# Kernel optimization log

Measured on AMD Instinct MI355X. Metric: run time of the kernel, lower is better.

Reference implementation:

```python
import jax, jax.numpy as jnp
import numpy as np
from functools import partial

V, E, H, F = 32000, 256, 512, 256  # vocab, embed_dim, hidden_dim, num_filters
FS = (3, 4, 5)

def setup_inputs() -> dict:
    key = jax.random.key(0)
    ks = jax.random.split(key, 24)
    s = 0.02
    d = {}
    d["src"] = jax.random.randint(ks[0], (32, 512), 0, V)
    d["trg"] = jax.random.randint(ks[1], (32, 64), 0, V)
    # embeddings with padding_idx=0 zeroed
    d["enc_emb"] = (jax.random.normal(ks[2], (V, E)) * s).at[0].set(0.0)
    d["dec_emb"] = (jax.random.normal(ks[3], (V, E)) * s).at[0].set(0.0)
    # conv1d weights (out_channels=F, in_channels=E, kernel)
    d["conv_w3"] = jax.random.normal(ks[4], (F, E, 3)) * s
    d["conv_b3"] = jnp.zeros((F,))
    d["conv_w4"] = jax.random.normal(ks[5], (F, E, 4)) * s
    d["conv_b4"] = jnp.zeros((F,))
    d["conv_w5"] = jax.random.normal(ks[6], (F, E, 5)) * s
    d["conv_b5"] = jnp.zeros((F,))
    d["fc1_w"] = jax.random.normal(ks[7], (H, 3 * F)) * s
    d["fc1_b"] = jnp.zeros((H,))
    d["fc2_w"] = jax.random.normal(ks[8], (H, H)) * s
    d["fc2_b"] = jnp.zeros((H,))
    # 2-layer LSTM: layer1 input E+H, layer2 input H; gates order i,f,g,o
    d["w_ih1"] = jax.random.normal(ks[9], (4 * H, E + H)) * s
    d["w_hh1"] = jax.random.normal(ks[10], (4 * H, H)) * s
    d["b_ih1"] = jnp.zeros((4 * H,))
    d["b_hh1"] = jnp.zeros((4 * H,))
    d["w_ih2"] = jax.random.normal(ks[11], (4 * H, H)) * s
    d["w_hh2"] = jax.random.normal(ks[12], (4 * H, H)) * s
    d["b_ih2"] = jnp.zeros((4 * H,))
    d["b_hh2"] = jnp.zeros((4 * H,))
    d["out_w"] = jax.random.normal(ks[13], (V, H)) * s
    d["out_b"] = jnp.zeros((V,))
    return d

def _lstm_cell(x, h, c, w_ih, w_hh, b_ih, b_hh):
    gates = x @ w_ih.T + b_ih + h @ w_hh.T + b_hh  # (B, 4H)
    i, f, g, o = jnp.split(gates, 4, axis=-1)
    c_new = jax.nn.sigmoid(f) * c + jax.nn.sigmoid(i) * jnp.tanh(g)
    h_new = jax.nn.sigmoid(o) * jnp.tanh(c_new)
    return h_new, c_new

def _encoder(src, enc_emb, convs, fc1_w, fc1_b, fc2_w, fc2_b):
    x = enc_emb[src]                    # (B, S, E)
    x = jnp.transpose(x, (0, 2, 1))     # (B, E, S)
    pooled = []
    for w, b in convs:
        y = jax.lax.conv_general_dilated(
            x, w, window_strides=(1,), padding='VALID',
            dimension_numbers=('NCH', 'OIH', 'NCH'))  # (B, F, S-k+1)
        pooled.append(jnp.max(jax.nn.relu(y + b[None, :, None]), axis=2))
    cat = jnp.concatenate(pooled, axis=1)              # (B, 3F)
    h = jax.nn.relu(cat @ fc1_w.T + fc1_b)             # (B, H)
    return h @ fc2_w.T + fc2_b                         # (B, H)

def reference(src, trg, enc_emb, conv_w3, conv_b3, conv_w4, conv_b4,
              conv_w5, conv_b5, fc1_w, fc1_b, fc2_w, fc2_b, dec_emb,
              w_ih1, w_hh1, b_ih1, b_hh1, w_ih2, w_hh2, b_ih2, b_hh2,
              out_w, out_b):
    B, T = trg.shape
    enc_out = _encoder(src, enc_emb,
                       [(conv_w3, conv_b3), (conv_w4, conv_b4), (conv_w5, conv_b5)],
                       fc1_w, fc1_b, fc2_w, fc2_b)  # (B, H)

    def step(carry, tok):
        h1, c1, h2, c2 = carry
        x = jnp.concatenate([dec_emb[tok], enc_out], axis=1)  # (B, E+H)
        h1, c1 = _lstm_cell(x, h1, c1, w_ih1, w_hh1, b_ih1, b_hh1)
        h2, c2 = _lstm_cell(h1, h2, c2, w_ih2, w_hh2, b_ih2, b_hh2)
        logits = h2 @ out_w.T + out_b                          # (B, V)
        return (h1, c1, h2, c2), logits

    z = jnp.zeros((B, H), dtype=enc_out.dtype)
    tokens = trg[:, :-1].T  # teacher forcing (ratio=1.0): (T-1, B)
    _, logits = jax.lax.scan(step, (z, z, z, z), tokens)       # (T-1, B, V)
    logits = jnp.transpose(logits, (1, 0, 2))                  # (B, T-1, V)
    # outputs[:, 0] is left as zeros, matching the torch loop starting at t=1
    return jnp.concatenate([jnp.zeros((B, 1, logits.shape[-1]), logits.dtype), logits], axis=1)
```

## Files before the change

kernel.cpp:

```cpp
#include <hip/hip_runtime.h>
#include <math.h>
#include <stdint.h>

#define B_    32
#define E_    256
#define F_    256
#define H_    512
#define V_    32000
#define G4    2048

typedef unsigned short u16;
typedef unsigned long long u64;
typedef __attribute__((ext_vector_type(8))) short bf16x8;
typedef __attribute__((ext_vector_type(4))) float f32x4;

__device__ __forceinline__ float fsig(float x) {
  return __builtin_amdgcn_rcpf(1.f + __expf(-x));
}
__device__ __forceinline__ float ftanh(float x) {
  return 1.f - 2.f * __builtin_amdgcn_rcpf(1.f + __expf(2.f * x));
}

__device__ __forceinline__ u16 f2bf(float f) {
  uint32_t u = __float_as_uint(f);
  uint32_t r = (u + 0x7FFFu + ((u >> 16) & 1u)) >> 16;
  return (u16)r;
}
__device__ __forceinline__ uint32_t pack2(float a, float b) {
  return (uint32_t)f2bf(a) | ((uint32_t)f2bf(b) << 16);
}

#define GLOAD16(gp, lp) __builtin_amdgcn_global_load_lds( \
    (const __attribute__((address_space(1))) uint32_t*)(const void*)(gp), \
    (__attribute__((address_space(3))) uint32_t*)(void*)(lp), 16, 0, 0)

#define ALOAD(P) __hip_atomic_load((P), __ATOMIC_RELAXED, __HIP_MEMORY_SCOPE_AGENT)
#define ASTORE(P, V) __hip_atomic_store((P), (V), __ATOMIC_RELAXED, __HIP_MEMORY_SCOPE_AGENT)

__global__ void prep_all(float* pooled, uint32_t* sent1, uint32_t* sent2,
                         uint32_t* cnt1, u16* h1d, u16* h2a,
                         const float* bi1, const float* bh1,
                         const float* bi2, const float* bh2,
                         float* bs1, float* bs2, float* out,
                         const float* s0, u16* d0, const float* s1, u16* d1,
                         const float* s2, u16* d2, const float* s3, u16* d3,
                         const float* s4, u16* d4,
                         const float* w3, u16* t3, const float* w4, u16* t4,
                         const float* w5, u16* t5) {
  int i = blockIdx.x * blockDim.x + threadIdx.x, st = gridDim.x * blockDim.x;
  for (int k = i; k < 2637824; k += st) {
    int j = k; const float* s; u16* d;
    if (j < 2048000) { s = s0; d = d0; }
    else if ((j -= 2048000) < 196608) { s = s1; d = d1; }
    else if ((j -= 196608) < 131072) { s = s2; d = d2; }
    else if ((j -= 131072) < 131072) { s = s3; d = d3; }
    else { j -= 131072; s = s4; d = d4; }
    const float4* sp = (const float4*)s + 2 * (size_t)j;
    float4 a = sp[0], b = sp[1];
    uint4 u;
    u.x = pack2(a.x, a.y); u.y = pack2(a.z, a.w);
    u.z = pack2(b.x, b.y); u.w = pack2(b.z, b.w);
    *((uint4*)d + j) = u;
  }
  for (int k = i; k < 786432; k += st) {
    int j = k; const float* w; u16* wt; int kw;
    if (j < 196608) { w = w3; wt = t3; kw = 3; }
    else if ((j -= 196608) < 262144) { w = w4; wt = t4; kw = 4; }
    else { j -= 262144; w = w5; wt = t5; kw = 5; }
    int f = j / (kw * 256);
    int r = j - f * (kw * 256);
    int jj = r >> 8, e = r & 255;
    wt[j] = f2bf(w[(f * 256 + e) * kw + jj]);
  }
  for (int k = i; k < 24576; k += st) pooled[k] = 0.f;
  for (int k = i; k < 131072; k += st) {
    uint32_t v = (k < 2048 && (k & 15) == 0) ? 1u : 0u;
    sent1[k] = v; sent2[k] = v;
  }
  for (int k = i; k < 256; k += st) cnt1[k] = 0u;
  uint4 z = {0u, 0u, 0u, 0u};
  for (int k = i; k < 2048; k += st) { ((uint4*)h1d)[k] = z; ((uint4*)h2a)[k] = z; }
  for (int k = i; k < G4; k += st) { bs1[k] = bi1[k] + bh1[k]; bs2[k] = bi2[k] + bh2[k]; }
  for (int k = i; k < B_ * V_; k += st) {
    int b = k / V_, v = k - b * V_;
    __builtin_nontemporal_store(0.f, &out[(size_t)b * 64 * V_ + v]);
  }
}

__global__ void gemm_small(const float* __restrict__ A, const float* __restrict__ W,
                           const float* __restrict__ bias, float* __restrict__ C,
                           int K, int N, int relu) {
  int nl = threadIdx.x & 7, b = threadIdx.x >> 3;
  int n = blockIdx.x * 8 + nl;
  const float* a = A + b * K;
  const float* w = W + (size_t)n * K;
  float acc = 0.f;
  for (int k = 0; k < K; k += 4) {
    float4 av = *reinterpret_cast<const float4*>(&a[k]);
    float4 wv = *reinterpret_cast<const float4*>(&w[k]);
    acc = fmaf(av.x, wv.x, acc); acc = fmaf(av.y, wv.y, acc);
    acc = fmaf(av.z, wv.z, acc); acc = fmaf(av.w, wv.w, acc);
  }
  acc += bias[n];
  if (relu) acc = fmaxf(acc, 0.f);
  C[b * N + n] = acc;
}

__global__ __launch_bounds__(256)
void conv_mfma(const u16* __restrict__ wt3, const u16* __restrict__ wt4,
               const u16* __restrict__ wt5,
               const float* __restrict__ cb3, const float* __restrict__ cb4,
               const float* __restrict__ cb5,
               float* __restrict__ pooled,
               const int* __restrict__ srcTok, const float* __restrict__ emb) {
  const int z = blockIdx.z;
  const u16* Bw = (z == 0) ? wt3 : (z == 1) ? wt4 : wt5;
  const float* bias = (z == 0) ? cb3 : (z == 1) ? cb4 : cb5;
  const int K = 768 + 256 * z, kw = 3 + z, poolOff = 256 * z;

  __shared__ char smem[32768];
  const int tid = threadIdx.x;
  const int wid = tid >> 6, lane = tid & 63;
  const int hi = lane >> 4, lo = lane & 15;
  const int wr = wid >> 1, wc = wid & 1;
  const int m0 = blockIdx.x * 128, n0 = blockIdx.y * 128;
  const int NT = K >> 5;
  const int srow = lane >> 2, sc = lane & 3;

  f32x4 acc[4][4];
#pragma unroll
  for (int i = 0; i < 4; ++i)
#pragma unroll
    for (int j = 0; j < 4; ++j) acc[i][j] = (f32x4){0.f, 0.f, 0.f, 0.f};

  for (int t = -1; t < NT; ++t) {
    int ts = t + 1;
    if (ts < NT) {
      char* base = smem + (ts & 1) * 16384;
      int k0 = ts << 5;
      {
        int j = k0 >> 8, e0 = k0 & 255;
        int row = tid >> 1;
        int m = m0 + row;
        int s = m & 511, b = m >> 9;
        int sj = s + j;
        int tok = (sj < 512) ? srcTok[b * 512 + sj] : -1;
#pragma unroll
        for (int q = 0; q < 2; ++q) {
          int cg = (tid & 1) * 2 + q;
          uint4 u;
          if (tok >= 0) {
            const float* ep = emb + (size_t)tok * 256 + e0 + cg * 8;
            float4 f0 = *(const float4*)(ep);
            float4 f1 = *(const float4*)(ep + 4);
            u.x = pack2(f0.x, f0.y); u.y = pack2(f0.z, f0.w);
            u.z = pack2(f1.x, f1.y); u.w = pack2(f1.z, f1.w);
          } else u = (uint4){0, 0, 0, 0};
          int c = cg ^ (row & 3);
          *(uint4*)(base + row * 64 + c * 16) = u;
        }
      }
#pragma unroll
      for (int q = 0; q < 2; ++q) {
        int row = (wid + q * 4) * 16 + srow;
        int gc = sc ^ (row & 3);
        const char* gp = (const char*)Bw + (((size_t)(n0 + row) * K + k0) << 1) + gc * 16;
        GLOAD16(gp, base + 8192 + (wid + q * 4) * 1024);
      }
    }
    if (t >= 0) {
      char* base = smem + (t & 1) * 16384;
      bf16x8 af[4], bfr[4];
#pragma unroll
      for (int mi = 0; mi < 4; ++mi) {
        int row = wr * 64 + mi * 16 + lo;
        af[mi] = *(const bf16x8*)(base + row * 64 + ((hi ^ (row & 3)) << 4));
      }
#pragma unroll
      for (int ni = 0; ni < 4; ++ni) {
        int row = wc * 64 + ni * 16 + lo;
        bfr[ni] = *(const bf16x8*)(base + 8192 + row * 64 + ((hi ^ (row & 3)) << 4));
      }
#pragma unroll
      for (int mi = 0; mi < 4; ++mi)
#pragma unroll
        for (int ni = 0; ni < 4; ++ni)
          acc[mi][ni] = __builtin_amdgcn_mfma_f32_16x16x32_bf16(af[mi], bfr[ni], acc[mi][ni], 0, 0, 0);
    }
    __syncthreads();
  }

  int b = m0 >> 9;
  int slim = 512 - kw;
#pragma unroll
  for (int ni = 0; ni < 4; ++ni) {
    int col = n0 + wc * 64 + ni * 16 + lo;
    float bv = bias[col];
    float mx = 0.f;
#pragma unroll
    for (int mi = 0; mi < 4; ++mi)
#pragma unroll
      for (int r = 0; r < 4; ++r) {
        int m = m0 + wr * 64 + mi * 16 + hi * 4 + r;
        int s = m & 511;
        float v = acc[mi][ni][r] + bv;
        if (s <= slim && v > mx) mx = v;
      }
    atomicMax((int*)&pooled[b * 768 + poolOff + col], __float_as_int(mx));
  }
}

__global__ __launch_bounds__(256, 1)
void lstm_fused(float* __restrict__ pre,
                const u16* __restrict__ whh1,
                const u16* __restrict__ wih2, const u16* __restrict__ whh2,
                const float* __restrict__ bs2,
                uint32_t* __restrict__ sent1, uint32_t* __restrict__ sent2,
                uint32_t* __restrict__ cnt1,
                u16* __restrict__ h1d, u16* __restrict__ h2a,
                const u16* __restrict__ outw_bf, const float* __restrict__ outb,
                float* __restrict__ out,
                const int* __restrict__ trg, const float* __restrict__ demb,
                const float* __restrict__ enco,
                const u16* __restrict__ wih1_bf, const float* __restrict__ bs1) {
  __shared__ char smem[74752];
  const int tid = threadIdx.x;
  const int wid = tid >> 6, lane = tid & 63, hi = lane >> 4, lo = lane & 15;
  const int hrow = tid >> 3, k8 = tid & 7;
  const int pb = hrow, pj0 = k8 * 2;

#define WAVE_DRAIN() asm volatile("s_waitcnt vmcnt(0)" ::: "memory")
#define POLL1(P) while (ALOAD(P) == 0u) __builtin_amdgcn_s_sleep(1);
#define POLL2(P, Q) for (;;) { uint32_t x_ = ALOAD(P), y_ = ALOAD(Q); \
                               if (x_ & y_) break; __builtin_amdgcn_s_sleep(1); }
#define POLL2S(P, Q) for (;;) { uint32_t x_ = ALOAD(P), y_ = ALOAD(Q); \
                                if (x_ & y_) break; __builtin_amdgcn_s_sleep(16); }

  if (blockIdx.x < 32) {
    const int bi = blockIdx.x;
    u16* hlds = (u16*)smem;
    float* glds = (float*)(smem + 33280);

    bf16x8 wreg[16];
    const u16* wp = whh1 + (((size_t)(wid * 512 + bi * 16 + lo)) << 9) + hi * 8;
#pragma unroll
    for (int ks = 0; ks < 16; ++ks) wreg[ks] = *(const bf16x8*)(wp + ks * 32);

    float creg0 = 0.f, creg1 = 0.f;

    for (int t = 0; t < 63; ++t) {
      if ((t & 3) == 0) {
        if (tid == 0)
          while (ALOAD(cnt1 + (t >> 2) * 16) < 16u) __builtin_amdgcn_s_sleep(8);
        __syncthreads();
      }
      const float* pr = pre + (((size_t)(t * 32 + pb)) << 11) + bi * 16 + pj0;
      float pi0 = pr[0], pf0 = pr[512], pg0 = pr[1024], po0 = pr[1536];
      float pi1 = pr[1], pf1 = pr[513], pg1 = pr[1025], po1 = pr[1537];

      const u64* hp = (const u64*)(h1d + ((size_t)t * 32 + hrow) * 512);
      f32x4 acc0 = (f32x4){0.f,0.f,0.f,0.f}, acc1 = (f32x4){0.f,0.f,0.f,0.f};

      POLL1(sent1 + (size_t)t * 2048 + lane * 16)
      {
        u64 v[8];
#pragma unroll
        for (int g = 0; g < 4; ++g) {
          int c = k8 + 8 * g;
          v[2*g]   = ALOAD(hp + 2 * c);
          v[2*g+1] = ALOAD(hp + 2 * c + 1);
        }
#pragma unroll
        for (int g = 0; g < 4; ++g) {
          int c = k8 + 8 * g;
          u64 w2[2] = { v[2*g], v[2*g+1] };
          *(uint4*)(hlds + hrow * 520 + c * 8) = *(const uint4*)w2;
        }
      }
      __syncthreads();
#pragma unroll
      for (int ks = 0; ks < 8; ++ks) {
        int cg = (ks * 4 + hi) * 8;
        bf16x8 a0 = *(const bf16x8*)(hlds + lo * 520 + cg);
        bf16x8 a1 = *(const bf16x8*)(hlds + (16 + lo) * 520 + cg);
        acc0 = __builtin_amdgcn_mfma_f32_16x16x32_bf16(a0, wreg[ks], acc0, 0, 0, 0);
        acc1 = __builtin_amdgcn_mfma_f32_16x16x32_bf16(a1, wreg[ks], acc1, 0, 0, 0);
      }
      POLL1(sent1 + (size_t)t * 2048 + (64 + lane) * 16)
      {
        u64 v[8];
#pragma unroll
        for (int g = 0; g < 4; ++g) {
          int c = 32 + k8 + 8 * g;
          v[2*g]   = ALOAD(hp + 2 * c);
          v[2*g+1] = ALOAD(hp + 2 * c + 1);
        }
#pragma unroll
        for (int g = 0; g < 4; ++g) {
          int c = 32 + k8 + 8 * g;
          u64 w2[2] = { v[2*g], v[2*g+1] };
          *(uint4*)(hlds + hrow * 520 + c * 8) = *(const uint4*)w2;
        }
      }
      __syncthreads();
#pragma unroll
      for (int ks = 8; ks < 16; ++ks) {
        int cg = (ks * 4 + hi) * 8;
        bf16x8 a0 = *(const bf16x8*)(hlds + lo * 520 + cg);
        bf16x8 a1 = *(const bf16x8*)(hlds + (16 + lo) * 520 + cg);
        acc0 = __builtin_amdgcn_mfma_f32_16x16x32_bf16(a0, wreg[ks], acc0, 0, 0, 0);
        acc1 = __builtin_amdgcn_mfma_f32_16x16x32_bf16(a1, wreg[ks], acc1, 0, 0, 0);
      }
#pragma unroll
      for (int r = 0; r < 4; ++r) {
        glds[wid * 544 + (hi * 4 + r) * 17 + lo] = acc0[r];
        glds[wid * 544 + (16 + hi * 4 + r) * 17 + lo] = acc1[r];
      }
      __syncthreads();

      float iv0 = glds[0*544 + pb*17 + pj0]   + pi0, fv0 = glds[1*544 + pb*17 + pj0]   + pf0;
      float gv0 = glds[2*544 + pb*17 + pj0]   + pg0, ov0 = glds[3*544 + pb*17 + pj0]   + po0;
      float iv1 = glds[0*544 + pb*17 + pj0+1] + pi1, fv1 = glds[1*544 + pb*17 + pj0+1] + pf1;
      float gv1 = glds[2*544 + pb*17 + pj0+1] + pg1, ov1 = glds[3*544 + pb*17 + pj0+1] + po1;
      float cn0 = fsig(fv0) * creg0 + fsig(iv0) * ftanh(gv0);
      float hn0 = fsig(ov0) * ftanh(cn0);
      float cn1 = fsig(fv1) * creg1 + fsig(iv1) * ftanh(gv1);
      float hn1 = fsig(ov1) * ftanh(cn1);
      creg0 = cn0; creg1 = cn1;
      ASTORE((uint32_t*)(h1d + ((size_t)(t + 1) * 32 + pb) * 512 + bi * 16 + pj0),
             pack2(hn0, hn1));
      WAVE_DRAIN();
      if (lane == 0)
        ASTORE(sent1 + (size_t)(t + 1) * 2048 + (bi * 4 + wid) * 16, 1u);
    }
  } else if (blockIdx.x < 64) {
    const int bi2 = blockIdx.x - 32;
    u16* alds = (u16*)smem;
    float* glds = (float*)(smem + 66048);

    bf16x8 wreg[32];
    {
      const u16* wa = wih2 + (((size_t)(wid * 512 + bi2 * 16 + lo)) << 9) + hi * 8;
      const u16* wb = whh2 + (((size_t)(wid * 512 + bi2 * 16 + lo)) << 9) + hi * 8;
#pragma unroll
      for (int ks = 0; ks < 16; ++ks) {
        wreg[ks]      = *(const bf16x8*)(wa + ks * 32);
        wreg[16 + ks] = *(const bf16x8*)(wb + ks * 32);
      }
    }
    float bsv0 = bs2[0 * 512 + bi2 * 16 + pj0], bsv0b = bs2[0 * 512 + bi2 * 16 + pj0 + 1];
    float bsv1 = bs2[1 * 512 + bi2 * 16 + pj0], bsv1b = bs2[1 * 512 + bi2 * 16 + pj0 + 1];
    float bsv2 = bs2[2 * 512 + bi2 * 16 + pj0], bsv2b = bs2[2 * 512 + bi2 * 16 + pj0 + 1];
    float bsv3 = bs2[3 * 512 + bi2 * 16 + pj0], bsv3b = bs2[3 * 512 + bi2 * 16 + pj0 + 1];

    float creg0 = 0.f, creg1 = 0.f;

    for (int t = 0; t < 63; ++t) {
      f32x4 acc0 = (f32x4){0.f,0.f,0.f,0.f}, acc1 = (f32x4){0.f,0.f,0.f,0.f};

      POLL2(sent1 + (size_t)(t + 1) * 2048 + lane * 16,
            sent1 + (size_t)(t + 1) * 2048 + (64 + lane) * 16)
      {
        const u64* hp1 = (const u64*)(h1d + ((size_t)(t + 1) * 32 + hrow) * 512);
        u64 v[16];
#pragma unroll
        for (int g = 0; g < 8; ++g) {
          int c = k8 + 8 * g;
          v[2*g]   = ALOAD(hp1 + 2 * c);
          v[2*g+1] = ALOAD(hp1 + 2 * c + 1);
        }
#pragma unroll
        for (int g = 0; g < 8; ++g) {
          int c = k8 + 8 * g;
          u64 w2[2] = { v[2*g], v[2*g+1] };
          *(uint4*)(alds + hrow * 1032 + c * 8) = *(const uint4*)w2;
        }
      }
      __syncthreads();
#pragma unroll
      for (int ks = 0; ks < 16; ++ks) {
        int cg = (ks * 4 + hi) * 8;
        bf16x8 a0 = *(const bf16x8*)(alds + lo * 1032 + cg);
        bf16x8 a1 = *(const bf16x8*)(alds + (16 + lo) * 1032 + cg);
        acc0 = __builtin_amdgcn_mfma_f32_16x16x32_bf16(a0, wreg[ks], acc0, 0, 0, 0);
        acc1 = __builtin_amdgcn_mfma_f32_16x16x32_bf16(a1, wreg[ks], acc1, 0, 0, 0);
      }
      POLL2(sent2 + (size_t)t * 2048 + lane * 16,
            sent2 + (size_t)t * 2048 + (64 + lane) * 16)
      {
        const u64* hp2 = (const u64*)(h2a + ((size_t)t * 32 + hrow) * 512);
        u64 v[16];
#pragma unroll
        for (int g = 0; g < 8; ++g) {
          int c = k8 + 8 * g;
          v[2*g]   = ALOAD(hp2 + 2 * c);
          v[2*g+1] = ALOAD(hp2 + 2 * c + 1);
        }
#pragma unroll
        for (int g = 0; g < 8; ++g) {
          int c = 64 + k8 + 8 * g;
          u64 w2[2] = { v[2*g], v[2*g+1] };
          *(uint4*)(alds + hrow * 1032 + c * 8) = *(const uint4*)w2;
        }
      }
      __syncthreads();
#pragma unroll
      for (int ks = 0; ks < 16; ++ks) {
        int cg = (64 + ks * 4 + hi) * 8;
        bf16x8 a0 = *(const bf16x8*)(alds + lo * 1032 + cg);
        bf16x8 a1 = *(const bf16x8*)(alds + (16 + lo) * 1032 + cg);
        acc0 = __builtin_amdgcn_mfma_f32_16x16x32_bf16(a0, wreg[16 + ks], acc0, 0, 0, 0);
        acc1 = __builtin_amdgcn_mfma_f32_16x16x32_bf16(a1, wreg[16 + ks], acc1, 0, 0, 0);
      }
#pragma unroll
      for (int r = 0; r < 4; ++r) {
        glds[wid * 544 + (hi * 4 + r) * 17 + lo] = acc0[r];
        glds[wid * 544 + (16 + hi * 4 + r) * 17 + lo] = acc1[r];
      }
      __syncthreads();

      float gi0 = glds[0*544 + pb*17 + pj0]   + bsv0,  gf0 = glds[1*544 + pb*17 + pj0]   + bsv1;
      float gg0 = glds[2*544 + pb*17 + pj0]   + bsv2,  go0 = glds[3*544 + pb*17 + pj0]   + bsv3;
      float gi1 = glds[0*544 + pb*17 + pj0+1] + bsv0b, gf1 = glds[1*544 + pb*17 + pj0+1] + bsv1b;
      float gg1 = glds[2*544 + pb*17 + pj0+1] + bsv2b, go1 = glds[3*544 + pb*17 + pj0+1] + bsv3b;
      float cn0 = fsig(gf0) * creg0 + fsig(gi0) * ftanh(gg0);
      float hn0 = fsig(go0) * ftanh(cn0);
      float cn1 = fsig(gf1) * creg1 + fsig(gi1) * ftanh(gg1);
      float hn1 = fsig(go1) * ftanh(cn1);
      creg0 = cn0; creg1 = cn1;
      ASTORE((uint32_t*)(h2a + ((size_t)(t + 1) * 32 + pb) * 512 + bi2 * 16 + pj0),
             pack2(hn0, hn1));
      WAVE_DRAIN();
      if (lane == 0)
        ASTORE(sent2 + (size_t)(t + 1) * 2048 + (bi2 * 4 + wid) * 16, 1u);
    }
  } else {
    const int bid2 = blockIdx.x - 64;
    const int wr = wid >> 1, wc = wid & 1;
    const int srow = lane >> 2, sc = lane & 3;

    for (int w = bid2; w < 256; w += 160) {
      int rt = w >> 4, ct = w & 15;
      const int m0 = rt * 128, n0 = ct * 128;
      f32x4 acc[4][4];
#pragma unroll
      for (int i = 0; i < 4; ++i)
#pragma unroll
        for (int j = 0; j < 4; ++j) acc[i][j] = (f32x4){0.f, 0.f, 0.f, 0.f};

      for (int t = -1; t < 24; ++t) {
        int ts = t + 1;
        if (ts < 24) {
          char* base = smem + (ts & 1) * 16384;
          int k0 = ts << 5;
          {
            int row = tid >> 1;
            int m = m0 + row;
            int tt = m >> 5, b = m & 31;
            int ok = (m < 2016);
            int tok = ok ? trg[b * 64 + tt] : 0;
#pragma unroll
            for (int q = 0; q < 2; ++q) {
              int cg = (tid & 1) * 2 + q;
              int k = k0 + cg * 8;
              uint4 u;
              if (ok) {
                const float* ep = (k < 256) ? (demb + (size_t)tok * 256 + k)
                                            : (enco + (size_t)b * 512 + (k - 256));
                float4 f0 = *(const float4*)(ep);
                float4 f1 = *(const float4*)(ep + 4);
                u.x = pack2(f0.x, f0.y); u.y = pack2(f0.z, f0.w);
                u.z = pack2(f1.x, f1.y); u.w = pack2(f1.z, f1.w);
              } else u = (uint4){0, 0, 0, 0};
              int c = cg ^ (row & 3);
              *(uint4*)(base + row * 64 + c * 16) = u;
            }
          }
#pragma unroll
          for (int q = 0; q < 2; ++q) {
            int row = (wid + q * 4) * 16 + srow;
            int gc = sc ^ (row & 3);
            const char* gp = (const char*)wih1_bf + (((size_t)(n0 + row) * 768 + k0) << 1) + gc * 16;
            GLOAD16(gp, base + 8192 + (wid + q * 4) * 1024);
          }
        }
        if (t >= 0) {
          char* base = smem + (t & 1) * 16384;
          bf16x8 af[4], bfr[4];
#pragma unroll
          for (int mi = 0; mi < 4; ++mi) {
            int row = wr * 64 + mi * 16 + lo;
            af[mi] = *(const bf16x8*)(base + row * 64 + ((hi ^ (row & 3)) << 4));
          }
#pragma unroll
          for (int ni = 0; ni < 4; ++ni) {
            int row = wc * 64 + ni * 16 + lo;
            bfr[ni] = *(const bf16x8*)(base + 8192 + row * 64 + ((hi ^ (row & 3)) << 4));
          }
#pragma unroll
          for (int mi = 0; mi < 4; ++mi)
#pragma unroll
            for (int ni = 0; ni < 4; ++ni)
              acc[mi][ni] = __builtin_amdgcn_mfma_f32_16x16x32_bf16(af[mi], bfr[ni], acc[mi][ni], 0, 0, 0);
        }
        __syncthreads();
      }
#pragma unroll
      for (int mi = 0; mi < 4; ++mi)
#pragma unroll
        for (int r = 0; r < 4; ++r) {
          int m = m0 + wr * 64 + mi * 16 + hi * 4 + r;
          if (m >= 2016) continue;
#pragma unroll
          for (int ni = 0; ni < 4; ++ni) {
            int col = n0 + wc * 64 + ni * 16 + lo;
            ASTORE((uint32_t*)(pre + (size_t)m * 2048 + col),
                   __float_as_uint(acc[mi][ni][r] + bs1[col]));
          }
        }
      WAVE_DRAIN();
      __syncthreads();
      if (tid == 0)
        __hip_atomic_fetch_add(cnt1 + rt * 16, 1u, __ATOMIC_RELAXED, __HIP_MEMORY_SCOPE_AGENT);
      __syncthreads();
    }

    const u16* A = h2a + 16384;

    for (int ct = bid2; ct < 250; ct += 160) {
      for (int rt = 0; rt < 16; ++rt) {
        int tf = rt * 4 + 4; if (tf > 63) tf = 63;
        if (wid == 0)
          POLL2S(sent2 + (size_t)tf * 2048 + lane * 16,
                 sent2 + (size_t)tf * 2048 + (64 + lane) * 16)
        __syncthreads();

        const int m0 = rt * 128, n0 = ct * 128;
        f32x4 acc[4][4];
#pragma unroll
        for (int i = 0; i < 4; ++i)
#pragma unroll
          for (int j = 0; j < 4; ++j) acc[i][j] = (f32x4){0.f, 0.f, 0.f, 0.f};

        for (int t = -1; t < 16; ++t) {
          int ts = t + 1;
          if (ts < 16) {
            char* base = smem + (ts & 1) * 16384;
            int k0 = ts << 5;
#pragma unroll
            for (int q = 0; q < 2; ++q) {
              int row = (wid + q * 4) * 16 + srow;
              int gc = sc ^ (row & 3);
              const char* gp = (const char*)A + (((size_t)(m0 + row) * 512 + k0) << 1) + gc * 16;
              GLOAD16(gp, base + (wid + q * 4) * 1024);
            }
#pragma unroll
            for (int q = 0; q < 2; ++q) {
              int row = (wid + q * 4) * 16 + srow;
              int gc = sc ^ (row & 3);
              const char* gp = (const char*)outw_bf + (((size_t)(n0 + row) * 512 + k0) << 1) + gc * 16;
              GLOAD16(gp, base + 8192 + (wid + q * 4) * 1024);
            }
          }
          if (t >= 0) {
            char* base = smem + (t & 1) * 16384;
            bf16x8 af[4], bfr[4];
#pragma unroll
            for (int mi = 0; mi < 4; ++mi) {
              int row = wr * 64 + mi * 16 + lo;
              af[mi] = *(const bf16x8*)(base + row * 64 + ((hi ^ (row & 3)) << 4));
            }
#pragma unroll
            for (int ni = 0; ni < 4; ++ni) {
              int row = wc * 64 + ni * 16 + lo;
              bfr[ni] = *(const bf16x8*)(base + 8192 + row * 64 + ((hi ^ (row & 3)) << 4));
            }
#pragma unroll
            for (int mi = 0; mi < 4; ++mi)
#pragma unroll
              for (int ni = 0; ni < 4; ++ni)
                acc[mi][ni] = __builtin_amdgcn_mfma_f32_16x16x32_bf16(af[mi], bfr[ni], acc[mi][ni], 0, 0, 0);
          }
          __syncthreads();
        }

#pragma unroll
        for (int mi = 0; mi < 4; ++mi)
#pragma unroll
          for (int r = 0; r < 4; ++r) {
            int m = m0 + wr * 64 + mi * 16 + hi * 4 + r;
            if (m >= 2016) continue;
            int t2 = m >> 5, b = m & 31;
            size_t rowbase = ((size_t)b * 64 + t2 + 1) * (size_t)V_;
#pragma unroll
            for (int ni = 0; ni < 4; ++ni) {
              int col = n0 + wc * 64 + ni * 16 + lo;
              __builtin_nontemporal_store(acc[mi][ni][r] + outb[col], &out[rowbase + col]);
            }
          }
      }
    }
  }
#undef POLL1
#undef POLL2
#undef POLL2S
#undef WAVE_DRAIN
}

extern "C" void kernel_launch(void* const* d_in, const int* in_sizes, int n_in,
                              void* d_out, int out_size, void* d_ws, size_t ws_size,
                              hipStream_t stream) {
  const int*   src  = (const int*)  d_in[0];
  const int*   trg  = (const int*)  d_in[1];
  const float* eemb = (const float*)d_in[2];
  const float* demb = (const float*)d_in[3];
  const float* cw3  = (const float*)d_in[4];
  const float* cb3  = (const float*)d_in[5];
  const float* cw4  = (const float*)d_in[6];
  const float* cb4  = (const float*)d_in[7];
  const float* cw5  = (const float*)d_in[8];
  const float* cb5  = (const float*)d_in[9];
  const float* fc1w = (const float*)d_in[10];
  const float* fc1b = (const float*)d_in[11];
  const float* fc2w = (const float*)d_in[12];
  const float* fc2b = (const float*)d_in[13];
  const float* wih1 = (const float*)d_in[14];
  const float* whh1 = (const float*)d_in[15];
  const float* bih1 = (const float*)d_in[16];
  const float* bhh1 = (const float*)d_in[17];
  const float* wih2 = (const float*)d_in[18];
  const float* whh2 = (const float*)d_in[19];
  const float* bih2 = (const float*)d_in[20];
  const float* bhh2 = (const float*)d_in[21];
  const float* outw = (const float*)d_in[22];
  const float* outb = (const float*)d_in[23];
  float* out = (float*)d_out;

  uint32_t* sent1 = (uint32_t*)d_ws;
  uint32_t* sent2 = sent1 + 131072;
  uint32_t* cnt1  = sent2 + 131072;
  u16* h1d      = (u16*)(cnt1 + 256);
  u16* h2a      = h1d + 1048576;
  float* pooled = (float*)(h2a + 1048576);
  float* ench   = pooled + 24576;
  float* enco   = ench + 16384;
  float* bs1    = enco + 16384;
  float* bs2    = bs1 + 2048;
  float* pre    = bs2 + 2048;
  u16* outw_bf  = (u16*)(pre + 4128768);
  u16* wih1_bf  = outw_bf + 16384000;
  u16* wih2_bf  = wih1_bf + 1572864;
  u16* whh1_bf  = wih2_bf + 1048576;
  u16* whh2_bf  = whh1_bf + 1048576;
  u16* wtj3     = whh2_bf + 1048576;
  u16* wtj4     = wtj3 + 196608;
  u16* wtj5     = wtj4 + 262144;

  prep_all<<<1024, 256, 0, stream>>>(pooled, sent1, sent2, cnt1, h1d, h2a,
                                     bih1, bhh1, bih2, bhh2, bs1, bs2, out,
                                     outw, outw_bf, wih1, wih1_bf, wih2, wih2_bf,
                                     whh1, whh1_bf, whh2, whh2_bf,
                                     cw3, wtj3, cw4, wtj4, cw5, wtj5);

  conv_mfma<<<dim3(128, 2, 3), 256, 0, stream>>>(wtj3, wtj4, wtj5, cb3, cb4, cb5,
                                                 pooled, src, eemb);
  gemm_small<<<64, 256, 0, stream>>>(pooled, fc1w, fc1b, ench, 768, 512, 1);
  gemm_small<<<64, 256, 0, stream>>>(ench, fc2w, fc2b, enco, 512, 512, 0);

  lstm_fused<<<224, 256, 0, stream>>>(pre, whh1_bf, wih2_bf, whh2_bf, bs2,
                                      sent1, sent2, cnt1, h1d, h2a,
                                      outw_bf, outb, out,
                                      trg, demb, enco, wih1_bf, bs1);
}
```

Measured before the change: 576.7 us.

## Pre-gather bf16 source embeddings, async-load conv A tiles, shrink fused LSTM grid

Gathers the source-token embeddings into a bf16 buffer once in the prep kernel, so the conv kernel can fill its A tiles with direct global-to-LDS loads (pointing out-of-range rows at a zero pad) instead of per-thread gather-and-convert. The fused LSTM kernel is launched with 160 blocks instead of 224, with 96 worker blocks, and the output-projection loop is reordered to sweep all column tiles per row band. Encoder-output reads become atomic loads. This cuts conv gather latency and may improve load balance, at the cost of an extra prep pass and fewer worker blocks.

```diff
diff --git a/kernel.cpp b/kernel.cpp
--- a/kernel.cpp
+++ b/kernel.cpp
@@ -8,6 +8,7 @@
 #define H_    512
 #define V_    32000
 #define G4    2048
+#define NWRK  96
 
 typedef unsigned short u16;
 typedef unsigned long long u64;
@@ -46,7 +47,8 @@
                          const float* s2, u16* d2, const float* s3, u16* d3,
                          const float* s4, u16* d4,
                          const float* w3, u16* t3, const float* w4, u16* t4,
-                         const float* w5, u16* t5) {
+                         const float* w5, u16* t5,
+                         const int* src, const float* eemb, u16* Xe, float* zpad) {
   int i = blockIdx.x * blockDim.x + threadIdx.x, st = gridDim.x * blockDim.x;
   for (int k = i; k < 2637824; k += st) {
     int j = k; const float* s; u16* d;
@@ -72,12 +74,23 @@
     int jj = r >> 8, e = r & 255;
     wt[j] = f2bf(w[(f * 256 + e) * kw + jj]);
   }
+  for (int j = i; j < 524288; j += st) {
+    int row = j >> 5, e0 = (j & 31) * 8;
+    int tok = src[row];
+    const float* ep = eemb + (size_t)tok * 256 + e0;
+    float4 a = *(const float4*)ep, b = *(const float4*)(ep + 4);
+    uint4 u;
+    u.x = pack2(a.x, a.y); u.y = pack2(a.z, a.w);
+    u.z = pack2(b.x, b.y); u.w = pack2(b.z, b.w);
+    *((uint4*)Xe + j) = u;
+  }
   for (int k = i; k < 24576; k += st) pooled[k] = 0.f;
   for (int k = i; k < 131072; k += st) {
     uint32_t v = (k < 2048 && (k & 15) == 0) ? 1u : 0u;
     sent1[k] = v; sent2[k] = v;
   }
   for (int k = i; k < 256; k += st) cnt1[k] = 0u;
+  for (int k = i; k < 16; k += st) zpad[k] = 0.f;
   uint4 z = {0u, 0u, 0u, 0u};
   for (int k = i; k < 2048; k += st) { ((uint4*)h1d)[k] = z; ((uint4*)h2a)[k] = z; }
   for (int k = i; k < G4; k += st) { bs1[k] = bi1[k] + bh1[k]; bs2[k] = bi2[k] + bh2[k]; }
@@ -112,7 +125,7 @@
                const float* __restrict__ cb3, const float* __restrict__ cb4,
                const float* __restrict__ cb5,
                float* __restrict__ pooled,
-               const int* __restrict__ srcTok, const float* __restrict__ emb) {
+               const u16* __restrict__ Xe, const float* __restrict__ zpad) {
   const int z = blockIdx.z;
   const u16* Bw = (z == 0) ? wt3 : (z == 1) ? wt4 : wt5;
   const float* bias = (z == 0) ? cb3 : (z == 1) ? cb4 : cb5;
@@ -138,27 +151,18 @@
     if (ts < NT) {
       char* base = smem + (ts & 1) * 16384;
       int k0 = ts << 5;
-      {
-        int j = k0 >> 8, e0 = k0 & 255;
-        int row = tid >> 1;
+      int j = k0 >> 8, e0 = k0 & 255;
+#pragma unroll
+      for (int q = 0; q < 2; ++q) {
+        int row = (wid + q * 4) * 16 + srow;
         int m = m0 + row;
         int s = m & 511, b = m >> 9;
         int sj = s + j;
-        int tok = (sj < 512) ? srcTok[b * 512 + sj] : -1;
-#pragma unroll
-        for (int q = 0; q < 2; ++q) {
-          int cg = (tid & 1) * 2 + q;
-          uint4 u;
-          if (tok >= 0) {
-            const float* ep = emb + (size_t)tok * 256 + e0 + cg * 8;
-            float4 f0 = *(const float4*)(ep);
-            float4 f1 = *(const float4*)(ep + 4);
-            u.x = pack2(f0.x, f0.y); u.y = pack2(f0.z, f0.w);
-            u.z = pack2(f1.x, f1.y); u.w = pack2(f1.z, f1.w);
-          } else u = (uint4){0, 0, 0, 0};
-          int c = cg ^ (row & 3);
-          *(uint4*)(base + row * 64 + c * 16) = u;
-        }
+        int gc = sc ^ (row & 3);
+        const char* gp = (sj < 512)
+            ? (const char*)(Xe + (((size_t)(b * 512 + sj)) << 8) + e0) + gc * 16
+            : (const char*)zpad;
+        GLOAD16(gp, base + (wid + q * 4) * 1024);
       }
 #pragma unroll
       for (int q = 0; q < 2; ++q) {
@@ -235,6 +239,8 @@
                                if (x_ & y_) break; __builtin_amdgcn_s_sleep(1); }
 #define POLL2S(P, Q) for (;;) { uint32_t x_ = ALOAD(P), y_ = ALOAD(Q); \
                                 if (x_ & y_) break; __builtin_amdgcn_s_sleep(16); }
+#define WAITCNT(P, TGT) { if (tid == 0) while (ALOAD(P) < (uint32_t)(TGT)) \
+                            __builtin_amdgcn_s_sleep(8); __syncthreads(); }
 
   if (blockIdx.x < 32) {
     const int bi = blockIdx.x;
@@ -249,11 +255,7 @@
     float creg0 = 0.f, creg1 = 0.f;
 
     for (int t = 0; t < 63; ++t) {
-      if ((t & 3) == 0) {
-        if (tid == 0)
-          while (ALOAD(cnt1 + (t >> 2) * 16) < 16u) __builtin_amdgcn_s_sleep(8);
-        __syncthreads();
-      }
+      if ((t & 3) == 0) WAITCNT(cnt1 + (t >> 2) * 16, 16)
       const float* pr = pre + (((size_t)(t * 32 + pb)) << 11) + bi * 16 + pj0;
       float pi0 = pr[0], pf0 = pr[512], pg0 = pr[1024], po0 = pr[1536];
       float pi1 = pr[1], pf1 = pr[513], pg1 = pr[1025], po1 = pr[1537];
@@ -439,7 +441,7 @@
     const int wr = wid >> 1, wc = wid & 1;
     const int srow = lane >> 2, sc = lane & 3;
 
-    for (int w = bid2; w < 256; w += 160) {
+    for (int w = bid2; w < 256; w += NWRK) {
       int rt = w >> 4, ct = w & 15;
       const int m0 = rt * 128, n0 = ct * 128;
       f32x4 acc[4][4];
@@ -463,15 +465,23 @@
             for (int q = 0; q < 2; ++q) {
               int cg = (tid & 1) * 2 + q;
               int k = k0 + cg * 8;
-              uint4 u;
+              uint4 u = {0, 0, 0, 0};
               if (ok) {
-                const float* ep = (k < 256) ? (demb + (size_t)tok * 256 + k)
-                                            : (enco + (size_t)b * 512 + (k - 256));
-                float4 f0 = *(const float4*)(ep);
-                float4 f1 = *(const float4*)(ep + 4);
-                u.x = pack2(f0.x, f0.y); u.y = pack2(f0.z, f0.w);
-                u.z = pack2(f1.x, f1.y); u.w = pack2(f1.z, f1.w);
-              } else u = (uint4){0, 0, 0, 0};
+                if (k < 256) {
+                  const float* ep = demb + (size_t)tok * 256 + k;
+                  float4 f0 = *(const float4*)(ep);
+                  float4 f1 = *(const float4*)(ep + 4);
+                  u.x = pack2(f0.x, f0.y); u.y = pack2(f0.z, f0.w);
+                  u.z = pack2(f1.x, f1.y); u.w = pack2(f1.z, f1.w);
+                } else {
+                  const u64* e2 = (const u64*)(enco + (size_t)b * 512 + (k - 256));
+                  u64 v0 = ALOAD(e2), v1 = ALOAD(e2 + 1), v2 = ALOAD(e2 + 2), v3 = ALOAD(e2 + 3);
+                  u.x = pack2(__uint_as_float((uint32_t)v0), __uint_as_float((uint32_t)(v0 >> 32)));
+                  u.y = pack2(__uint_as_float((uint32_t)v1), __uint_as_float((uint32_t)(v1 >> 32)));
+                  u.z = pack2(__uint_as_float((uint32_t)v2), __uint_as_float((uint32_t)(v2 >> 32)));
+                  u.w = pack2(__uint_as_float((uint32_t)v3), __uint_as_float((uint32_t)(v3 >> 32)));
+                }
+              }
               int c = cg ^ (row & 3);
               *(uint4*)(base + row * 64 + c * 16) = u;
             }
@@ -527,8 +537,9 @@
 
     const u16* A = h2a + 16384;
 
-    for (int ct = bid2; ct < 250; ct += 160) {
-      for (int rt = 0; rt < 16; ++rt) {
+    for (int rtb = 0; rtb < 4; ++rtb) {
+      for (int w = bid2; w < 1000; w += NWRK) {
+        int rt = rtb * 4 + w / 250, ct = w - (w / 250) * 250;
         int tf = rt * 4 + 4; if (tf > 63) tf = 63;
         if (wid == 0)
           POLL2S(sent2 + (size_t)tf * 2048 + lane * 16,
@@ -604,6 +615,7 @@
 #undef POLL1
 #undef POLL2
 #undef POLL2S
+#undef WAITCNT
 #undef WAVE_DRAIN
 }
 
@@ -646,7 +658,8 @@
   float* enco   = ench + 16384;
   float* bs1    = enco + 16384;
   float* bs2    = bs1 + 2048;
-  float* pre    = bs2 + 2048;
+  float* zpad   = bs2 + 2048;
+  float* pre    = zpad + 16;
   u16* outw_bf  = (u16*)(pre + 4128768);
   u16* wih1_bf  = outw_bf + 16384000;
   u16* wih2_bf  = wih1_bf + 1572864;
@@ -655,19 +668,21 @@
   u16* wtj3     = whh2_bf + 1048576;
   u16* wtj4     = wtj3 + 196608;
   u16* wtj5     = wtj4 + 262144;
+  u16* Xe       = wtj5 + 327680;
 
   prep_all<<<1024, 256, 0, stream>>>(pooled, sent1, sent2, cnt1, h1d, h2a,
                                      bih1, bhh1, bih2, bhh2, bs1, bs2, out,
                                      outw, outw_bf, wih1, wih1_bf, wih2, wih2_bf,
                                      whh1, whh1_bf, whh2, whh2_bf,
-                                     cw3, wtj3, cw4, wtj4, cw5, wtj5);
+                                     cw3, wtj3, cw4, wtj4, cw5, wtj5,
+                                     src, eemb, Xe, zpad);
 
   conv_mfma<<<dim3(128, 2, 3), 256, 0, stream>>>(wtj3, wtj4, wtj5, cb3, cb4, cb5,
-                                                 pooled, src, eemb);
+                                                 pooled, Xe, zpad);
   gemm_small<<<64, 256, 0, stream>>>(pooled, fc1w, fc1b, ench, 768, 512, 1);
   gemm_small<<<64, 256, 0, stream>>>(ench, fc2w, fc2b, enco, 512, 512, 0);
 
-  lstm_fused<<<224, 256, 0, stream>>>(pre, whh1_bf, wih2_bf, whh2_bf, bs2,
+  lstm_fused<<<160, 256, 0, stream>>>(pre, whh1_bf, wih2_bf, whh2_bf, bs2,
                                       sent1, sent2, cnt1, h1d, h2a,
                                       outw_bf, outb, out,
                                       trg, demb, enco, wih1_bf, bs1);
```

New measurement: 671.3 us. 16.4% more time.
